# Performance work log

Measured on AMD Instinct MI355X. Metric: run time of the kernel, lower is better.

The kernel has to match this reference:

```python
import jax, jax.numpy as jnp
import numpy as np

GRID_SIZE = 5
GRID_RANGE = (-1.0, 1.0)


def setup_inputs() -> dict:
    key = jax.random.key(0)
    k1, k2, k3 = jax.random.split(key, 3)
    B, D, U, K = 16384, 1024, 128, GRID_SIZE + 3  # spline_order=3
    x = jax.random.normal(k1, (B, D), dtype=jnp.float32)
    # glorot-ish scale for weights
    base_weight = jax.random.normal(k2, (D, U), dtype=jnp.float32) * (1.0 / np.sqrt(D))
    spline_weight = jax.random.normal(k3, (D, U, K), dtype=jnp.float32) * (1.0 / np.sqrt(D))
    return {"x": x, "base_weight": base_weight, "spline_weight": spline_weight}


def reference(x, base_weight, spline_weight):
    # base path: SiLU(x @ W_b)
    base_out = jax.nn.silu(x @ base_weight)  # [B, U]
    # spline path: RBF over grid centers, then contract (note: x_norm in the
    # original call() is computed but unused, so it is omitted here)
    centers = jnp.linspace(GRID_RANGE[0], GRID_RANGE[1], GRID_SIZE)  # [G]
    dist = jnp.square(x[..., None] - centers)        # [B, D, G]
    rbf = jnp.exp(-5.0 * dist)                        # [B, D, G]
    spline_out = jnp.einsum('big,iug->bu', rbf, spline_weight[:, :, :GRID_SIZE])
    return base_out + spline_out
```

## Files before the change

### kernel.cpp

```cpp
#include <hip/hip_runtime.h>

typedef unsigned short u16;
typedef unsigned int u32;
typedef __bf16 bf16x8 __attribute__((ext_vector_type(8)));
typedef float f32x16 __attribute__((ext_vector_type(16)));

#define C2 (-7.213475204444817f)
#define T1C 0.28650480f
#define T2C 0.0067379470f

__device__ __forceinline__ u16 f2bf(float f) {
  u32 u = __float_as_uint(f);
  return (u16)((u + 0x7FFFu + ((u >> 16) & 1u)) >> 16);
}

__device__ __forceinline__ f32x16 mfma16(uint4 a, uint4 b, f32x16 c) {
  return __builtin_amdgcn_mfma_f32_32x32x16_bf16(
      __builtin_bit_cast(bf16x8, a), __builtin_bit_cast(bf16x8, b), c, 0, 0, 0);
}

__global__ __launch_bounds__(256) void kan_prep(const float* __restrict__ wb,
                                                const float* __restrict__ ws,
                                                u16* __restrict__ wst3) {
  __shared__ u16 tile[6][16][130];
  const int t = threadIdx.x;
  const int c = blockIdx.x;
#pragma unroll
  for (int it = 0; it < 8; ++it) {
    int idx = it * 256 + t;
    int d = idx >> 7, u = idx & 127;
    size_t base = (size_t)(c * 16 + d) * 128 + u;
    const float* p = ws + base * 8;
    float4 v0 = *(const float4*)p;
    float g4 = p[4];
    tile[0][d][u] = f2bf(v0.x);
    tile[1][d][u] = f2bf(v0.y);
    tile[2][d][u] = f2bf(v0.z);
    tile[3][d][u] = f2bf(v0.w);
    tile[4][d][u] = f2bf(g4);
    tile[5][d][u] = f2bf(wb[base]);
  }
  __syncthreads();
#pragma unroll
  for (int i = 0; i < 6; ++i) {
    int g = i * 256 + t;
    int s = g >> 8, r = g & 255;
    int nq = r >> 6, l = r & 63;
    int u = nq * 32 + (l & 31);
    int dbase = (l >> 5) * 8;
    u32 q[4];
#pragma unroll
    for (int j = 0; j < 4; ++j) {
      u32 lo = tile[s][dbase + 2 * j][u];
      u32 hi = tile[s][dbase + 2 * j + 1][u];
      q[j] = lo | (hi << 16);
    }
    uint4 w4; w4.x = q[0]; w4.y = q[1]; w4.z = q[2]; w4.w = q[3];
    *(uint4*)(wst3 + (size_t)c * 12288 + (size_t)g * 8) = w4;
  }
}

__global__ __launch_bounds__(512, 2) void kan_main(const float* __restrict__ x,
                                                   const u16* __restrict__ wst3,
                                                   float* __restrict__ out) {
  __shared__ __align__(16) char lds[65536];

  const int t = threadIdx.x;
  const int lane = t & 63;
  const int w = t >> 6;
  const int kq = w & 3;
  const int wn = w >> 2;
  const int b0 = blockIdx.x * 64;

  f32x16 acc[8];
#pragma unroll
  for (int i = 0; i < 8; ++i)
#pragma unroll
    for (int j = 0; j < 16; ++j) acc[i][j] = 0.f;

  const int srow = t >> 3, sq = t & 7;
  const float* xsrc =
      x + (size_t)(b0 + srow) * 1024 + (size_t)((sq ^ (srow & 7)) * 4);

  auto stage = [&](char* buf, int body) {
    const float* s0 = xsrc + body * 32;
#pragma unroll
    for (int rr = 0; rr < 4; ++rr) {
      __builtin_amdgcn_global_load_lds(
          (const __attribute__((address_space(1))) u32*)(s0 + rr * 256),
          (__attribute__((address_space(3))) u32*)(buf + rr * 8192 + w * 1024),
          16, 0, 0);
    }
  };

  const int rrow = lane & 31;
  const int kh = lane >> 5;
  const int rs = rrow & 7;

  const char* bsrc =
      (const char*)wst3 + (size_t)kq * 393216 + wn * 2048 + lane * 16;

  auto mkfrag = [&](const float4& xa, const float4& xb, uint4* fr) {
    float xf[8] = {xa.x, xa.y, xa.z, xa.w, xb.x, xb.y, xb.z, xb.w};
    u32 pk[6][4];
#pragma unroll
    for (int pp = 0; pp < 4; ++pp) {
      u32 lo6[6], hi6[6];
#pragma unroll
      for (int e = 0; e < 2; ++e) {
        float xv = xf[2 * pp + e];
        float t0 = C2 * xv;
        float P = __builtin_amdgcn_exp2f(t0 * xv);
        float Qp = __builtin_amdgcn_exp2f(-t0);
        float Qm = __builtin_amdgcn_exp2f(t0);
        float PQ = P * Qp, PQm = P * Qm;
        u32* dst = e ? hi6 : lo6;
        dst[0] = __float_as_uint(PQm * Qm * T2C) + 0x8000u;
        dst[1] = __float_as_uint(PQm * T1C) + 0x8000u;
        dst[2] = __float_as_uint(P) + 0x8000u;
        dst[3] = __float_as_uint(PQ * T1C) + 0x8000u;
        dst[4] = __float_as_uint(PQ * Qp * T2C) + 0x8000u;
        dst[5] = __float_as_uint(xv) + 0x8000u;
      }
#pragma unroll
      for (int s = 0; s < 6; ++s)
        pk[s][pp] = __builtin_amdgcn_perm(hi6[s], lo6[s], 0x07060302);
    }
#pragma unroll
    for (int s = 0; s < 6; ++s) {
      fr[s].x = pk[s][0]; fr[s].y = pk[s][1];
      fr[s].z = pk[s][2]; fr[s].w = pk[s][3];
    }
  };

  stage(lds, 0);
  __syncthreads();

  for (int i = 0; i < 8; ++i) {
    char* cur = lds + (i & 1) * 32768;
    char* nxt = lds + ((i + 1) & 1) * 32768;
    if (i < 7) stage(nxt, i + 1);

#pragma unroll
    for (int cc = 0; cc < 2; ++cc) {
      const char* bc = bsrc + (size_t)(i * 2 + cc) * 24576;
      uint4 b0v[6], b1v[6];
#pragma unroll
      for (int s = 0; s < 6; ++s) {
        b0v[s] = *(const uint4*)(bc + s * 4096);
        b1v[s] = *(const uint4*)(bc + s * 4096 + 1024);
      }
      const char* wbase = cur + kq * 8192;
      const int q0 = cc * 4 + kh * 2;
      const int sA = q0 ^ rs, sB = (q0 + 1) ^ rs;
      const char* r0 = wbase + rrow * 128;
      const char* r1 = wbase + (32 + rrow) * 128;
      float4 xa0 = *(const float4*)(r0 + sA * 16);
      float4 xb0 = *(const float4*)(r0 + sB * 16);
      float4 xa1 = *(const float4*)(r1 + sA * 16);
      float4 xb1 = *(const float4*)(r1 + sB * 16);
      uint4 fa[6], fb[6];
      mkfrag(xa0, xb0, fa);
      mkfrag(xa1, xb1, fb);
#pragma unroll
      for (int s = 0; s < 5; ++s) {
        acc[0] = mfma16(fa[s], b0v[s], acc[0]);
        acc[1] = mfma16(fa[s], b1v[s], acc[1]);
        acc[2] = mfma16(fb[s], b0v[s], acc[2]);
        acc[3] = mfma16(fb[s], b1v[s], acc[3]);
      }
      acc[4] = mfma16(fa[5], b0v[5], acc[4]);
      acc[5] = mfma16(fa[5], b1v[5], acc[5]);
      acc[6] = mfma16(fb[5], b0v[5], acc[6]);
      acc[7] = mfma16(fb[5], b1v[5], acc[7]);
    }
    __syncthreads();
  }

#pragma unroll
  for (int q = 0; q < 4; ++q) {
    if (kq != 0) {
      char* slab = lds + ((kq - 1) * 2 + wn) * 8192;
#pragma unroll
      for (int rq = 0; rq < 4; ++rq) {
        *(float4*)(slab + rq * 1024 + lane * 16) =
            make_float4(acc[q][4 * rq], acc[q][4 * rq + 1],
                        acc[q][4 * rq + 2], acc[q][4 * rq + 3]);
        *(float4*)(slab + 4096 + rq * 1024 + lane * 16) =
            make_float4(acc[4 + q][4 * rq], acc[4 + q][4 * rq + 1],
                        acc[4 + q][4 * rq + 2], acc[4 + q][4 * rq + 3]);
      }
    }
    __syncthreads();
    if (kq == 0) {
#pragma unroll
      for (int p = 1; p < 4; ++p) {
        const char* slab = lds + ((p - 1) * 2 + wn) * 8192;
#pragma unroll
        for (int rq = 0; rq < 4; ++rq) {
          float4 vs = *(const float4*)(slab + rq * 1024 + lane * 16);
          float4 vb = *(const float4*)(slab + 4096 + rq * 1024 + lane * 16);
          acc[q][4 * rq] += vs.x; acc[q][4 * rq + 1] += vs.y;
          acc[q][4 * rq + 2] += vs.z; acc[q][4 * rq + 3] += vs.w;
          acc[4 + q][4 * rq] += vb.x; acc[4 + q][4 * rq + 1] += vb.y;
          acc[4 + q][4 * rq + 2] += vb.z; acc[4 + q][4 * rq + 3] += vb.w;
        }
      }
      const int col = wn * 64 + (q & 1) * 32 + (lane & 31);
#pragma unroll
      for (int reg = 0; reg < 16; ++reg) {
        int row = (q >> 1) * 32 + (reg & 3) + 8 * (reg >> 2) + 4 * (lane >> 5);
        float z = acc[4 + q][reg];
        float sv = z / (1.0f + __expf(-z));
        out[(size_t)(b0 + row) * 128 + col] = sv + acc[q][reg];
      }
    }
    __syncthreads();
  }
}

extern "C" void kernel_launch(void* const* d_in, const int* in_sizes, int n_in,
                              void* d_out, int out_size, void* d_ws, size_t ws_size,
                              hipStream_t stream) {
  const float* x  = (const float*)d_in[0];
  const float* wb = (const float*)d_in[1];
  const float* ws = (const float*)d_in[2];
  u16* wst3 = (u16*)d_ws;
  float* out = (float*)d_out;

  kan_prep<<<dim3(64), 256, 0, stream>>>(wb, ws, wst3);
  kan_main<<<dim3(256), 512, 0, stream>>>(x, wst3, out);
}
```

Before: 137.2 us.

## Load x directly into registers and software-pipeline B fragment prefetch across split-K waves

Restructures the main kernel so that each wave owns a 32-row M tile, a 64-column N slice and half of K. Activations are read straight from global memory into registers instead of being staged through LDS with global_load_lds. The weight fragments for the next chunk are prefetched into registers in two halves interleaved with the MFMAs. This removes the per-iteration LDS staging and barriers and shrinks the cross-wave reduction to a single two-way reduction. The risk is higher register pressure, weaker global load coalescing for x, and a loss of x reuse across waves, since each wave now covers fewer rows per B fragment.

```diff
diff --git a/kernel.cpp b/kernel.cpp
--- a/kernel.cpp
+++ b/kernel.cpp
@@ -68,37 +68,26 @@
   const int t = threadIdx.x;
   const int lane = t & 63;
   const int w = t >> 6;
-  const int kq = w & 3;
-  const int wn = w >> 2;
+  const int kc = w >> 2;
+  const int wn = (w >> 1) & 1;
+  const int wm = w & 1;
   const int b0 = blockIdx.x * 64;
-
-  f32x16 acc[8];
-#pragma unroll
-  for (int i = 0; i < 8; ++i)
-#pragma unroll
-    for (int j = 0; j < 16; ++j) acc[i][j] = 0.f;
-
-  const int srow = t >> 3, sq = t & 7;
-  const float* xsrc =
-      x + (size_t)(b0 + srow) * 1024 + (size_t)((sq ^ (srow & 7)) * 4);
-
-  auto stage = [&](char* buf, int body) {
-    const float* s0 = xsrc + body * 32;
-#pragma unroll
-    for (int rr = 0; rr < 4; ++rr) {
-      __builtin_amdgcn_global_load_lds(
-          (const __attribute__((address_space(1))) u32*)(s0 + rr * 256),
-          (__attribute__((address_space(3))) u32*)(buf + rr * 8192 + w * 1024),
-          16, 0, 0);
-    }
+  const int m = lane & 31, kh = lane >> 5;
+
+  const float* xp = x + (size_t)(b0 + wm * 32 + m) * 1024 + kc * 512 + kh * 8;
+  const char* bp = (const char*)wst3 + (size_t)kc * 32 * 24576 + wn * 2048 +
+                   (size_t)lane * 16;
+
+  f32x16 sp0, sp1, ba0, ba1;
+#pragma unroll
+  for (int i = 0; i < 16; ++i) { sp0[i] = 0.f; sp1[i] = 0.f; ba0[i] = 0.f; ba1[i] = 0.f; }
+
+  uint4 bA[6], bB[6];
+  float4 xw[8];
+
+  auto ldb = [&](int chunk, int s, int q) {
+    return *(const uint4*)(bp + (size_t)chunk * 24576 + s * 4096 + q * 1024);
   };
-
-  const int rrow = lane & 31;
-  const int kh = lane >> 5;
-  const int rs = rrow & 7;
-
-  const char* bsrc =
-      (const char*)wst3 + (size_t)kq * 393216 + wn * 2048 + lane * 16;
 
   auto mkfrag = [&](const float4& xa, const float4& xb, uint4* fr) {
     float xf[8] = {xa.x, xa.y, xa.z, xa.w, xb.x, xb.y, xb.z, xb.w};
@@ -133,89 +122,100 @@
     }
   };
 
-  stage(lds, 0);
+  auto body = [&](int j, bool refillB, bool refillX, int w2, int ci) {
+    uint4 fa[6];
+    mkfrag(xw[2 * ci], xw[2 * ci + 1], fa);
+    if (refillX) {
+#pragma unroll
+      for (int c2 = 0; c2 < 4; ++c2) {
+        xw[2 * c2] = *(const float4*)(xp + (w2 + 1) * 64 + c2 * 16);
+        xw[2 * c2 + 1] = *(const float4*)(xp + (w2 + 1) * 64 + c2 * 16 + 4);
+      }
+    }
+#pragma unroll
+    for (int s = 0; s < 3; ++s) {
+      sp0 = mfma16(fa[s], bA[2 * s], sp0);
+      sp1 = mfma16(fa[s], bA[2 * s + 1], sp1);
+    }
+    if (refillB) {
+#pragma unroll
+      for (int s = 0; s < 3; ++s) {
+        bA[2 * s] = ldb(j + 1, s, 0);
+        bA[2 * s + 1] = ldb(j + 1, s, 1);
+      }
+    }
+    sp0 = mfma16(fa[3], bB[0], sp0);
+    sp1 = mfma16(fa[3], bB[1], sp1);
+    sp0 = mfma16(fa[4], bB[2], sp0);
+    sp1 = mfma16(fa[4], bB[3], sp1);
+    ba0 = mfma16(fa[5], bB[4], ba0);
+    ba1 = mfma16(fa[5], bB[5], ba1);
+    if (refillB) {
+#pragma unroll
+      for (int s = 0; s < 3; ++s) {
+        bB[2 * s] = ldb(j + 1, s + 3, 0);
+        bB[2 * s + 1] = ldb(j + 1, s + 3, 1);
+      }
+    }
+  };
+
+#pragma unroll
+  for (int ci = 0; ci < 4; ++ci) {
+    xw[2 * ci] = *(const float4*)(xp + ci * 16);
+    xw[2 * ci + 1] = *(const float4*)(xp + ci * 16 + 4);
+  }
+#pragma unroll
+  for (int s = 0; s < 3; ++s) {
+    bA[2 * s] = ldb(0, s, 0);
+    bA[2 * s + 1] = ldb(0, s, 1);
+    bB[2 * s] = ldb(0, s + 3, 0);
+    bB[2 * s + 1] = ldb(0, s + 3, 1);
+  }
+
+  for (int w2 = 0; w2 < 7; ++w2) {
+#pragma unroll
+    for (int ci = 0; ci < 4; ++ci) body(w2 * 4 + ci, true, ci == 3, w2, ci);
+  }
+#pragma unroll
+  for (int ci = 0; ci < 4; ++ci) body(28 + ci, ci < 3, false, 7, ci);
+
+  char* slab = lds + (wm * 2 + wn) * 16384;
+  if (kc == 1) {
+#pragma unroll
+    for (int rq = 0; rq < 4; ++rq) {
+      *(float4*)(slab + 0 * 4096 + rq * 1024 + lane * 16) =
+          make_float4(sp0[4 * rq], sp0[4 * rq + 1], sp0[4 * rq + 2], sp0[4 * rq + 3]);
+      *(float4*)(slab + 1 * 4096 + rq * 1024 + lane * 16) =
+          make_float4(sp1[4 * rq], sp1[4 * rq + 1], sp1[4 * rq + 2], sp1[4 * rq + 3]);
+      *(float4*)(slab + 2 * 4096 + rq * 1024 + lane * 16) =
+          make_float4(ba0[4 * rq], ba0[4 * rq + 1], ba0[4 * rq + 2], ba0[4 * rq + 3]);
+      *(float4*)(slab + 3 * 4096 + rq * 1024 + lane * 16) =
+          make_float4(ba1[4 * rq], ba1[4 * rq + 1], ba1[4 * rq + 2], ba1[4 * rq + 3]);
+    }
+  }
   __syncthreads();
-
-  for (int i = 0; i < 8; ++i) {
-    char* cur = lds + (i & 1) * 32768;
-    char* nxt = lds + ((i + 1) & 1) * 32768;
-    if (i < 7) stage(nxt, i + 1);
-
-#pragma unroll
-    for (int cc = 0; cc < 2; ++cc) {
-      const char* bc = bsrc + (size_t)(i * 2 + cc) * 24576;
-      uint4 b0v[6], b1v[6];
-#pragma unroll
-      for (int s = 0; s < 6; ++s) {
-        b0v[s] = *(const uint4*)(bc + s * 4096);
-        b1v[s] = *(const uint4*)(bc + s * 4096 + 1024);
-      }
-      const char* wbase = cur + kq * 8192;
-      const int q0 = cc * 4 + kh * 2;
-      const int sA = q0 ^ rs, sB = (q0 + 1) ^ rs;
-      const char* r0 = wbase + rrow * 128;
-      const char* r1 = wbase + (32 + rrow) * 128;
-      float4 xa0 = *(const float4*)(r0 + sA * 16);
-      float4 xb0 = *(const float4*)(r0 + sB * 16);
-      float4 xa1 = *(const float4*)(r1 + sA * 16);
-      float4 xb1 = *(const float4*)(r1 + sB * 16);
-      uint4 fa[6], fb[6];
-      mkfrag(xa0, xb0, fa);
-      mkfrag(xa1, xb1, fb);
-#pragma unroll
-      for (int s = 0; s < 5; ++s) {
-        acc[0] = mfma16(fa[s], b0v[s], acc[0]);
-        acc[1] = mfma16(fa[s], b1v[s], acc[1]);
-        acc[2] = mfma16(fb[s], b0v[s], acc[2]);
-        acc[3] = mfma16(fb[s], b1v[s], acc[3]);
-      }
-      acc[4] = mfma16(fa[5], b0v[5], acc[4]);
-      acc[5] = mfma16(fa[5], b1v[5], acc[5]);
-      acc[6] = mfma16(fb[5], b0v[5], acc[6]);
-      acc[7] = mfma16(fb[5], b1v[5], acc[7]);
-    }
-    __syncthreads();
-  }
-
-#pragma unroll
-  for (int q = 0; q < 4; ++q) {
-    if (kq != 0) {
-      char* slab = lds + ((kq - 1) * 2 + wn) * 8192;
-#pragma unroll
-      for (int rq = 0; rq < 4; ++rq) {
-        *(float4*)(slab + rq * 1024 + lane * 16) =
-            make_float4(acc[q][4 * rq], acc[q][4 * rq + 1],
-                        acc[q][4 * rq + 2], acc[q][4 * rq + 3]);
-        *(float4*)(slab + 4096 + rq * 1024 + lane * 16) =
-            make_float4(acc[4 + q][4 * rq], acc[4 + q][4 * rq + 1],
-                        acc[4 + q][4 * rq + 2], acc[4 + q][4 * rq + 3]);
-      }
-    }
-    __syncthreads();
-    if (kq == 0) {
-#pragma unroll
-      for (int p = 1; p < 4; ++p) {
-        const char* slab = lds + ((p - 1) * 2 + wn) * 8192;
-#pragma unroll
-        for (int rq = 0; rq < 4; ++rq) {
-          float4 vs = *(const float4*)(slab + rq * 1024 + lane * 16);
-          float4 vb = *(const float4*)(slab + 4096 + rq * 1024 + lane * 16);
-          acc[q][4 * rq] += vs.x; acc[q][4 * rq + 1] += vs.y;
-          acc[q][4 * rq + 2] += vs.z; acc[q][4 * rq + 3] += vs.w;
-          acc[4 + q][4 * rq] += vb.x; acc[4 + q][4 * rq + 1] += vb.y;
-          acc[4 + q][4 * rq + 2] += vb.z; acc[4 + q][4 * rq + 3] += vb.w;
-        }
-      }
-      const int col = wn * 64 + (q & 1) * 32 + (lane & 31);
-#pragma unroll
-      for (int reg = 0; reg < 16; ++reg) {
-        int row = (q >> 1) * 32 + (reg & 3) + 8 * (reg >> 2) + 4 * (lane >> 5);
-        float z = acc[4 + q][reg];
-        float sv = z / (1.0f + __expf(-z));
-        out[(size_t)(b0 + row) * 128 + col] = sv + acc[q][reg];
-      }
-    }
-    __syncthreads();
+  if (kc == 0) {
+#pragma unroll
+    for (int rq = 0; rq < 4; ++rq) {
+      float4 v0 = *(const float4*)(slab + 0 * 4096 + rq * 1024 + lane * 16);
+      float4 v1 = *(const float4*)(slab + 1 * 4096 + rq * 1024 + lane * 16);
+      float4 v2 = *(const float4*)(slab + 2 * 4096 + rq * 1024 + lane * 16);
+      float4 v3 = *(const float4*)(slab + 3 * 4096 + rq * 1024 + lane * 16);
+      sp0[4 * rq] += v0.x; sp0[4 * rq + 1] += v0.y; sp0[4 * rq + 2] += v0.z; sp0[4 * rq + 3] += v0.w;
+      sp1[4 * rq] += v1.x; sp1[4 * rq + 1] += v1.y; sp1[4 * rq + 2] += v1.z; sp1[4 * rq + 3] += v1.w;
+      ba0[4 * rq] += v2.x; ba0[4 * rq + 1] += v2.y; ba0[4 * rq + 2] += v2.z; ba0[4 * rq + 3] += v2.w;
+      ba1[4 * rq] += v3.x; ba1[4 * rq + 1] += v3.y; ba1[4 * rq + 2] += v3.z; ba1[4 * rq + 3] += v3.w;
+    }
+#pragma unroll
+    for (int reg = 0; reg < 16; ++reg) {
+      int row = wm * 32 + (reg & 3) + 8 * (reg >> 2) + 4 * (lane >> 5);
+      float z0 = ba0[reg];
+      float z1 = ba1[reg];
+      float s0 = z0 / (1.0f + __expf(-z0));
+      float s1 = z1 / (1.0f + __expf(-z1));
+      out[(size_t)(b0 + row) * 128 + wn * 64 + 0 * 32 + (lane & 31)] = s0 + sp0[reg];
+      out[(size_t)(b0 + row) * 128 + wn * 64 + 1 * 32 + (lane & 31)] = s1 + sp1[reg];
+    }
   }
 }
 
```

Result: slower. 153.4 us (+11.9%).
